# Performance work log

Hardware: AMD Instinct MI355X
Metric: run time of the kernel (lower is better)

The kernel has to match this reference:

```python
import jax, jax.numpy as jnp
import numpy as np

NUM_HEADS = 8


def setup_inputs() -> dict:
    key = jax.random.key(0)
    k1, k2, k3 = jax.random.split(key, 3)
    B, L, E, H = 4, 2048, 256, NUM_HEADS
    x = jax.random.normal(k1, (B, L, E), dtype=jnp.float32)
    W_qkv = jax.random.normal(k2, (E, H * E * 3), dtype=jnp.float32) * 0.02
    W_out = jax.random.normal(k3, (H * E, E), dtype=jnp.float32) * 0.02
    return {"x": x, "W_qkv": W_qkv, "W_out": W_out}


def reference(x, W_qkv, W_out):
    B, L, E = x.shape
    H = NUM_HEADS
    qkv = x @ W_qkv  # [B, L, 3*H*E]
    q, k, v = jnp.split(qkv, 3, axis=-1)  # each [B, L, H*E]
    # reshape(B, L, H, E) then move heads before sequence -> [B, H, L, E]
    q = q.reshape(B, L, H, E).transpose(0, 2, 1, 3)
    k = k.reshape(B, L, H, E).transpose(0, 2, 1, 3)
    v = v.reshape(B, L, H, E).transpose(0, 2, 1, 3)
    scale = 1.0 / jnp.sqrt(jnp.asarray(E, dtype=x.dtype))
    scores = jnp.einsum("bhqe,bhke->bhqk", q, k) * scale  # [B, H, L, L]
    attn = jax.nn.softmax(scores, axis=-1)
    out = jnp.einsum("bhqk,bhke->bhqe", attn, v)  # [B, H, L, E]
    out = out.transpose(0, 2, 1, 3).reshape(B, L, H * E)
    return out @ W_out  # [B, L, E]
```

## Files before the change

kernel.cpp:

```cpp
#include <hip/hip_runtime.h>
#include <cstdint>
#include <cstddef>

typedef __bf16 bf16_t;
typedef __bf16 bf16x8 __attribute__((ext_vector_type(8)));
typedef __bf16 bf16x4 __attribute__((ext_vector_type(4)));
typedef float  f32x4  __attribute__((ext_vector_type(4)));
typedef float  f32x16 __attribute__((ext_vector_type(16)));

#define MFMA16(a, b, c) __builtin_amdgcn_mfma_f32_16x16x32_bf16((a), (b), (c), 0, 0, 0)
#define MFMA32(a, b, c) __builtin_amdgcn_mfma_f32_32x32x16_bf16((a), (b), (c), 0, 0, 0)
#define CVTPK(d, a, b) \
  asm("v_cvt_pk_bf16_f32 %0, %1, %2" : "=v"(d) : "v"(a), "v"(b))
#define PLSWAP(a, b) \
  asm("v_permlane32_swap_b32 %0, %1" : "+v"(a), "+v"(b))

__device__ __forceinline__ void gload_lds16(const bf16_t* g, bf16_t* l) {
  __builtin_amdgcn_global_load_lds(
      (__attribute__((address_space(1))) void*)((void*)g),
      (__attribute__((address_space(3))) void*)l, 16, 0, 0);
}

__global__ __launch_bounds__(256) void cvt_f32_bf16(
    const float* __restrict__ in, bf16_t* __restrict__ out, int n) {
  const int i = (blockIdx.x * 256 + threadIdx.x) * 4;
  if (i + 3 < n) {
    const float4 v = *(const float4*)(in + i);
    bf16x4 o;
    o[0] = (bf16_t)v.x; o[1] = (bf16_t)v.y; o[2] = (bf16_t)v.z; o[3] = (bf16_t)v.w;
    *(bf16x4*)(out + i) = o;
  }
}

__global__ __launch_bounds__(256) void transpose_f32_bf16(
    const float* __restrict__ in, bf16_t* __restrict__ out, int R, int C) {
  __shared__ bf16_t tile[32][33];
  const int bc = blockIdx.x * 32, br = blockIdx.y * 32;
  const int tx = threadIdx.x, ty = threadIdx.y;
#pragma unroll
  for (int i = 0; i < 32; i += 8)
    tile[ty + i][tx] = (bf16_t)in[(size_t)(br + ty + i) * C + bc + tx];
  __syncthreads();
#pragma unroll
  for (int i = 0; i < 32; i += 8)
    out[(size_t)(bc + ty + i) * R + br + tx] = tile[tx][ty + i];
}

template <int EPI>
__global__ __launch_bounds__(256) void gemm_bt(
    const bf16_t* __restrict__ A, const bf16_t* __restrict__ Bt,
    void* __restrict__ Cout, bf16_t* __restrict__ Vt, int M, int N, int K) {
  __shared__ __align__(16) bf16_t As[128 * 32];
  __shared__ __align__(16) bf16_t Bs[128 * 32];
  const int tid = threadIdx.x;
  const int lane = tid & 63, w = tid >> 6;
  const int wm = w >> 1, wn = w & 1;
  const int bm = blockIdx.y * 128, bn = blockIdx.x * 128;
  const int l15 = lane & 15, l4 = lane >> 4;

  f32x4 acc[4][4] = {};

  for (int k0 = 0; k0 < K; k0 += 32) {
    __syncthreads();
#pragma unroll
    for (int i = 0; i < 2; ++i) {
      const int idx = i * 256 + tid;
      const int r = idx >> 2, s = idx & 3;
      const int ss = s ^ (r & 3);
      gload_lds16(A + (size_t)(bm + r) * K + k0 + ss * 8, &As[idx * 8]);
      gload_lds16(Bt + (size_t)(bn + r) * K + k0 + ss * 8, &Bs[idx * 8]);
    }
    __syncthreads();
    bf16x8 af[4], bfr[4];
#pragma unroll
    for (int f = 0; f < 4; ++f) {
      const int ra = wm * 64 + f * 16 + l15;
      const int rb = wn * 64 + f * 16 + l15;
      af[f]  = *(const bf16x8*)&As[ra * 32 + (l4 ^ (ra & 3)) * 8];
      bfr[f] = *(const bf16x8*)&Bs[rb * 32 + (l4 ^ (rb & 3)) * 8];
    }
#pragma unroll
    for (int i = 0; i < 4; ++i)
#pragma unroll
      for (int j = 0; j < 4; ++j) acc[i][j] = MFMA16(af[i], bfr[j], acc[i][j]);
  }

#pragma unroll
  for (int i = 0; i < 4; ++i) {
    const int gr = bm + wm * 64 + i * 16 + l4 * 4;
#pragma unroll
    for (int j = 0; j < 4; ++j) {
      const int gc = bn + wn * 64 + j * 16 + l15;
      if constexpr (EPI == 0) {
        float* C = (float*)Cout;
#pragma unroll
        for (int r = 0; r < 4; ++r)
          C[(size_t)(gr + r) * N + gc] = acc[i][j][r];
      } else {
        bf16_t* C = (bf16_t*)Cout;
        if (gc < 2048) {
#pragma unroll
          for (int r = 0; r < 4; ++r)
            C[(size_t)(gr + r) * 4096 + gc] = (bf16_t)(acc[i][j][r] * 0.0625f);
        } else if (gc < 4096) {
#pragma unroll
          for (int r = 0; r < 4; ++r)
            C[(size_t)(gr + r) * 4096 + gc] = (bf16_t)acc[i][j][r];
        } else {
          const int c = gc - 4096, h = c >> 8, d = c & 255;
          const int b = gr >> 11, lt = gr & 2047;
          bf16x4 pk;
#pragma unroll
          for (int r = 0; r < 4; ++r) pk[r] = (bf16_t)acc[i][j][r];
          *(bf16x4*)&Vt[((size_t)(b * 8 + h) * 256 + d) * 2048 + lt] = pk;
        }
      }
    }
  }
}

__global__ __launch_bounds__(256, 1) void attn_fwd(
    const bf16_t* __restrict__ qk, const bf16_t* __restrict__ vt,
    bf16_t* __restrict__ ao) {
  __shared__ __align__(16) bf16_t Ks[2][64 * 256];
  __shared__ __align__(16) bf16_t Vs[2][256 * 64];
  const int tid = threadIdx.x, lane = tid & 63, w = tid >> 6;
  const int l31 = lane & 31, h5 = lane >> 5, p3 = l31 & 7;
  const int bid = blockIdx.x;
  const int swz = (bid & 7) * 64 + (bid >> 3);
  const int qt = swz & 15;
  const int bh = swz >> 4;
  const int bb = bh >> 3, hh = bh & 7;

  const int qcol = qt * 128 + w * 32 + l31;
  const bf16_t* qbase =
      qk + (size_t)(bb * 2048 + qcol) * 4096 + hh * 256 + h5 * 8;
  bf16x8 qf[16];
#pragma unroll
  for (int s = 0; s < 16; ++s) qf[s] = *(const bf16x8*)(qbase + s * 16);

  const bf16_t* kg = qk + (size_t)(bb * 2048) * 4096 + 2048 + hh * 256;
  const bf16_t* vg = vt + (size_t)bh * 256 * 2048;

#define STAGE_TILES(bufidx, tile)                                           \
  {                                                                         \
    const int t64 = (tile) * 64;                                            \
    _Pragma("unroll") for (int c = 0; c < 8; ++c) {                         \
      const int idx = c * 256 + tid;                                        \
      const int kr = idx >> 5, kse = idx & 31;                              \
      gload_lds16(kg + (size_t)(t64 + kr) * 4096 + ((kse ^ (kr & 7)) * 8),  \
                  &Ks[bufidx][idx * 8]);                                    \
    }                                                                       \
    _Pragma("unroll") for (int c = 0; c < 8; ++c) {                         \
      const int idx = c * 256 + tid;                                        \
      const int vr = idx >> 3, vse = idx & 7;                               \
      gload_lds16(vg + (size_t)vr * 2048 + t64 + ((vse ^ (vr & 7)) * 8),    \
                  &Vs[bufidx][idx * 8]);                                    \
    }                                                                       \
  }

  STAGE_TILES(0, 0);
  STAGE_TILES(1, 1);

  f32x16 o[8] = {};
  float m = -1e30f, lsum = 0.f;

  for (int kv = 0; kv < 32; ++kv) {
    const int cur = kv & 1;
    asm volatile("s_waitcnt vmcnt(16)" ::: "memory");
    __builtin_amdgcn_s_barrier();
    __builtin_amdgcn_sched_barrier(0);
    const bf16_t* Kc = Ks[cur];
    const bf16_t* Vc = Vs[cur];

    f32x16 sa0 = {}, sa1 = {};
    __builtin_amdgcn_s_setprio(1);
#pragma unroll
    for (int s = 0; s < 16; ++s) {
      const int so = ((2 * s + h5) ^ p3) << 4;
      bf16x8 kf0 = *(const bf16x8*)((const char*)Kc + l31 * 512 + so);
      bf16x8 kf1 = *(const bf16x8*)((const char*)Kc + (32 + l31) * 512 + so);
      sa0 = MFMA32(kf0, qf[s], sa0);
      sa1 = MFMA32(kf1, qf[s], sa1);
    }
    __builtin_amdgcn_s_setprio(0);

    float pm = sa0[0];
#pragma unroll
    for (int r = 1; r < 16; ++r) pm = fmaxf(pm, sa0[r]);
#pragma unroll
    for (int r = 0; r < 16; ++r) pm = fmaxf(pm, sa1[r]);
    pm = fmaxf(pm, __shfl_xor(pm, 32));
    if (!__all(pm <= m)) {
      const float mn = fmaxf(m, pm);
      const float al = __expf(m - mn);
      m = mn;
      lsum *= al;
#pragma unroll
      for (int dt = 0; dt < 8; ++dt)
#pragma unroll
        for (int r = 0; r < 16; ++r) o[dt][r] *= al;
    }
    float rs = 0.f;
#pragma unroll
    for (int r = 0; r < 16; ++r) { sa0[r] = __expf(sa0[r] - m); rs += sa0[r]; }
#pragma unroll
    for (int r = 0; r < 16; ++r) { sa1[r] = __expf(sa1[r] - m); rs += sa1[r]; }
    rs += __shfl_xor(rs, 32);
    lsum += rs;

    __builtin_amdgcn_s_setprio(1);
#define PV_KSTEP(SA, c0, s2)                                                \
    {                                                                       \
      unsigned w0, w1, w2, w3;                                              \
      CVTPK(w0, SA[4 * (c0) + 0], SA[4 * (c0) + 1]);                        \
      CVTPK(w2, SA[4 * (c0) + 4], SA[4 * (c0) + 5]);                        \
      PLSWAP(w0, w2);                                                       \
      CVTPK(w1, SA[4 * (c0) + 2], SA[4 * (c0) + 3]);                        \
      CVTPK(w3, SA[4 * (c0) + 6], SA[4 * (c0) + 7]);                        \
      PLSWAP(w1, w3);                                                       \
      union { unsigned u[4]; bf16x8 v; } pu;                                \
      pu.u[0] = w0; pu.u[1] = w1; pu.u[2] = w2; pu.u[3] = w3;               \
      _Pragma("unroll") for (int dt = 0; dt < 8; ++dt) {                    \
        bf16x8 vf = *(const bf16x8*)((const char*)Vc +                      \
            (dt * 32 + l31) * 128 + (((2 * (s2) + h5) ^ p3) << 4));         \
        o[dt] = MFMA32(vf, pu.v, o[dt]);                                    \
      }                                                                     \
    }
    PV_KSTEP(sa0, 0, 0);
    PV_KSTEP(sa0, 2, 1);
    PV_KSTEP(sa1, 0, 2);
    PV_KSTEP(sa1, 2, 3);
    __builtin_amdgcn_s_setprio(0);

    __builtin_amdgcn_sched_barrier(0);
    __builtin_amdgcn_s_barrier();
    __builtin_amdgcn_sched_barrier(0);
    STAGE_TILES(cur, (kv + 2) & 31);
  }

  const float inv = 1.0f / lsum;
  bf16_t* aor = ao + (size_t)(bb * 2048 + qcol) * 2048 + hh * 256 + 4 * h5;
#pragma unroll
  for (int dt = 0; dt < 8; ++dt)
#pragma unroll
    for (int c = 0; c < 4; ++c) {
      bf16x4 ov;
#pragma unroll
      for (int bq = 0; bq < 4; ++bq) ov[bq] = (bf16_t)(o[dt][4 * c + bq] * inv);
      *(bf16x4*)(aor + dt * 32 + 8 * c) = ov;
    }
}

extern "C" void kernel_launch(void* const* d_in, const int* in_sizes, int n_in,
                              void* d_out, int out_size, void* d_ws,
                              size_t ws_size, hipStream_t stream) {
  (void)in_sizes; (void)n_in; (void)out_size; (void)ws_size;
  const float* x    = (const float*)d_in[0];
  const float* wqkv = (const float*)d_in[1];
  const float* wout = (const float*)d_in[2];
  float* out = (float*)d_out;

  char* ws = (char*)d_ws;
  bf16_t* xb  = (bf16_t*)(ws);
  bf16_t* wqt = (bf16_t*)(ws + 4194304);
  bf16_t* wot = (bf16_t*)(ws + 7340032);
  bf16_t* qkb = (bf16_t*)(ws + 8388608);
  bf16_t* vtb = (bf16_t*)(ws + 8388608 + 67108864);
  bf16_t* aob = (bf16_t*)(ws + 8388608 + 67108864 + 33554432);

  cvt_f32_bf16<<<2048, 256, 0, stream>>>(x, xb, 8192 * 256);
  transpose_f32_bf16<<<dim3(192, 8), dim3(32, 8), 0, stream>>>(wqkv, wqt, 256, 6144);
  transpose_f32_bf16<<<dim3(8, 64), dim3(32, 8), 0, stream>>>(wout, wot, 2048, 256);
  gemm_bt<1><<<dim3(48, 64), 256, 0, stream>>>(xb, wqt, qkb, vtb, 8192, 6144, 256);
  attn_fwd<<<512, 256, 0, stream>>>(qkb, vtb, aob);
  gemm_bt<0><<<dim3(2, 64), 256, 0, stream>>>(aob, wot, out, nullptr, 8192, 256, 2048);
}
```

Before: 344.4 us.

## Halve attention KV tile to 32 to fit two blocks per CU

Shrinks the K/V LDS tiles from 64 to 32 keys so shared memory per block halves, and raises launch bounds to request two blocks per CU. The swizzle patterns and the PV k-steps are adapted to the narrower tile, and the loop runs 64 iterations. The intent is better latency hiding through co-resident workgroups. The cost is more barriers and softmax bookkeeping per key, plus a tighter register budget that may cause spills given the large accumulator and Q fragment arrays.

Result: no change. 346.0 us (+0.4%).

```diff
diff --git a/kernel.cpp b/kernel.cpp
--- a/kernel.cpp
+++ b/kernel.cpp
@@ -119,13 +119,14 @@
   }
 }
 
-__global__ __launch_bounds__(256, 1) void attn_fwd(
+__global__ __launch_bounds__(256, 2) void attn_fwd(
     const bf16_t* __restrict__ qk, const bf16_t* __restrict__ vt,
     bf16_t* __restrict__ ao) {
-  __shared__ __align__(16) bf16_t Ks[2][64 * 256];
-  __shared__ __align__(16) bf16_t Vs[2][256 * 64];
+  __shared__ __align__(16) bf16_t Ks[2][32 * 256];
+  __shared__ __align__(16) bf16_t Vs[2][256 * 32];
   const int tid = threadIdx.x, lane = tid & 63, w = tid >> 6;
-  const int l31 = lane & 31, h5 = lane >> 5, p3 = l31 & 7;
+  const int l31 = lane & 31, h5 = lane >> 5;
+  const int p4 = l31 & 15, p2 = l31 & 3;
   const int bid = blockIdx.x;
   const int swz = (bid & 7) * 64 + (bid >> 3);
   const int qt = swz & 15;
@@ -144,17 +145,17 @@
 
 #define STAGE_TILES(bufidx, tile)                                           \
   {                                                                         \
-    const int t64 = (tile) * 64;                                            \
-    _Pragma("unroll") for (int c = 0; c < 8; ++c) {                         \
+    const int t32 = (tile) * 32;                                            \
+    _Pragma("unroll") for (int c = 0; c < 4; ++c) {                         \
       const int idx = c * 256 + tid;                                        \
       const int kr = idx >> 5, kse = idx & 31;                              \
-      gload_lds16(kg + (size_t)(t64 + kr) * 4096 + ((kse ^ (kr & 7)) * 8),  \
+      gload_lds16(kg + (size_t)(t32 + kr) * 4096 + ((kse ^ (kr & 15)) * 8), \
                   &Ks[bufidx][idx * 8]);                                    \
     }                                                                       \
-    _Pragma("unroll") for (int c = 0; c < 8; ++c) {                         \
+    _Pragma("unroll") for (int c = 0; c < 4; ++c) {                         \
       const int idx = c * 256 + tid;                                        \
-      const int vr = idx >> 3, vse = idx & 7;                               \
-      gload_lds16(vg + (size_t)vr * 2048 + t64 + ((vse ^ (vr & 7)) * 8),    \
+      const int vr = idx >> 2, vse = idx & 3;                               \
+      gload_lds16(vg + (size_t)vr * 2048 + t32 + ((vse ^ (vr & 3)) * 8),    \
                   &Vs[bufidx][idx * 8]);                                    \
     }                                                                       \
   }
@@ -165,31 +166,27 @@
   f32x16 o[8] = {};
   float m = -1e30f, lsum = 0.f;
 
-  for (int kv = 0; kv < 32; ++kv) {
+  for (int kv = 0; kv < 64; ++kv) {
     const int cur = kv & 1;
-    asm volatile("s_waitcnt vmcnt(16)" ::: "memory");
+    asm volatile("s_waitcnt vmcnt(8)" ::: "memory");
     __builtin_amdgcn_s_barrier();
     __builtin_amdgcn_sched_barrier(0);
     const bf16_t* Kc = Ks[cur];
     const bf16_t* Vc = Vs[cur];
 
-    f32x16 sa0 = {}, sa1 = {};
+    f32x16 sa = {};
     __builtin_amdgcn_s_setprio(1);
 #pragma unroll
     for (int s = 0; s < 16; ++s) {
-      const int so = ((2 * s + h5) ^ p3) << 4;
-      bf16x8 kf0 = *(const bf16x8*)((const char*)Kc + l31 * 512 + so);
-      bf16x8 kf1 = *(const bf16x8*)((const char*)Kc + (32 + l31) * 512 + so);
-      sa0 = MFMA32(kf0, qf[s], sa0);
-      sa1 = MFMA32(kf1, qf[s], sa1);
+      bf16x8 kf = *(const bf16x8*)
+          ((const char*)Kc + l31 * 512 + (((2 * s + h5) ^ p4) << 4));
+      sa = MFMA32(kf, qf[s], sa);
     }
     __builtin_amdgcn_s_setprio(0);
 
-    float pm = sa0[0];
-#pragma unroll
-    for (int r = 1; r < 16; ++r) pm = fmaxf(pm, sa0[r]);
-#pragma unroll
-    for (int r = 0; r < 16; ++r) pm = fmaxf(pm, sa1[r]);
+    float pm = sa[0];
+#pragma unroll
+    for (int r = 1; r < 16; ++r) pm = fmaxf(pm, sa[r]);
     pm = fmaxf(pm, __shfl_xor(pm, 32));
     if (!__all(pm <= m)) {
       const float mn = fmaxf(m, pm);
@@ -203,9 +200,7 @@
     }
     float rs = 0.f;
 #pragma unroll
-    for (int r = 0; r < 16; ++r) { sa0[r] = __expf(sa0[r] - m); rs += sa0[r]; }
-#pragma unroll
-    for (int r = 0; r < 16; ++r) { sa1[r] = __expf(sa1[r] - m); rs += sa1[r]; }
+    for (int r = 0; r < 16; ++r) { sa[r] = __expf(sa[r] - m); rs += sa[r]; }
     rs += __shfl_xor(rs, 32);
     lsum += rs;
 
@@ -223,20 +218,18 @@
       pu.u[0] = w0; pu.u[1] = w1; pu.u[2] = w2; pu.u[3] = w3;               \
       _Pragma("unroll") for (int dt = 0; dt < 8; ++dt) {                    \
         bf16x8 vf = *(const bf16x8*)((const char*)Vc +                      \
-            (dt * 32 + l31) * 128 + (((2 * (s2) + h5) ^ p3) << 4));         \
+            (dt * 32 + l31) * 64 + ((((s2) * 2 + h5) ^ p2) << 4));          \
         o[dt] = MFMA32(vf, pu.v, o[dt]);                                    \
       }                                                                     \
     }
-    PV_KSTEP(sa0, 0, 0);
-    PV_KSTEP(sa0, 2, 1);
-    PV_KSTEP(sa1, 0, 2);
-    PV_KSTEP(sa1, 2, 3);
+    PV_KSTEP(sa, 0, 0);
+    PV_KSTEP(sa, 2, 1);
     __builtin_amdgcn_s_setprio(0);
 
     __builtin_amdgcn_sched_barrier(0);
     __builtin_amdgcn_s_barrier();
     __builtin_amdgcn_sched_barrier(0);
-    STAGE_TILES(cur, (kv + 2) & 31);
+    STAGE_TILES(cur, (kv + 2) & 63);
   }
 
   const float inv = 1.0f / lsum;
```
